# Optimization experiments

Measured on AMD Instinct MI355X. Metric: run time of the kernel, lower is better.

Reference implementation:

```python
import jax, jax.numpy as jnp
import numpy as np

B, N, M = 1, 3000, 3000        # surface points, query points
K = N + M                       # nodes per graph
IN, HID, H, OUT = 3, 64, 4, 2   # in_channels, hidden_channels, heads, out_channels
RADIUS2 = 0.05 ** 2
NEG_SLOPE = 0.2
NEG_INF = jnp.float32(-1e9)


def setup_inputs() -> dict:
    key = jax.random.key(0)
    ks = jax.random.split(key, 12)
    s1 = 1.0 / np.sqrt(IN)
    s2 = 1.0 / np.sqrt(H * HID)
    return {
        "pos": jax.random.uniform(ks[0], (B, 3, N), dtype=jnp.float32),
        "pos_non_manifold": jax.random.uniform(ks[1], (B, 3, M), dtype=jnp.float32),
        # GAT layer 1: lin weight, attention vectors (per head), bias
        "W1": jax.random.normal(ks[2], (IN, H * HID), dtype=jnp.float32) * s1,
        "a_src1": jax.random.normal(ks[3], (H, HID), dtype=jnp.float32) * s2,
        "a_dst1": jax.random.normal(ks[4], (H, HID), dtype=jnp.float32) * s2,
        "b1": jnp.zeros((H * HID,), dtype=jnp.float32),
        # GAT layer 2
        "W2": jax.random.normal(ks[5], (H * HID, H * HID), dtype=jnp.float32) * s2,
        "a_src2": jax.random.normal(ks[6], (H, HID), dtype=jnp.float32) * s2,
        "a_dst2": jax.random.normal(ks[7], (H, HID), dtype=jnp.float32) * s2,
        "b2": jnp.zeros((H * HID,), dtype=jnp.float32),
        # final fc
        "fc_w": jax.random.normal(ks[8], (H * HID, OUT), dtype=jnp.float32) * s2,
        "fc_b": jnp.zeros((OUT,), dtype=jnp.float32),
    }


def _gat_layer(x, mask, W, a_src, a_dst, b):
    # x: [B,K,Fin]; mask: [B,K,K] (mask[b,i,j] True if edge j->i, symmetric, incl. diag)
    h = (x @ W).reshape(x.shape[0], x.shape[1], H, HID)        # [B,K,H,C]
    es = jnp.einsum('bjhc,hc->bjh', h, a_src)                   # source score
    ed = jnp.einsum('bihc,hc->bih', h, a_dst)                   # destination score
    e = ed[:, :, None, :] + es[:, None, :, :]                   # [B,i,j,H]
    e = jnp.where(e >= 0, e, NEG_SLOPE * e)                     # LeakyReLU(0.2)
    e = jnp.where(mask[..., None], e, NEG_INF)
    alpha = jax.nn.softmax(e, axis=2)                           # softmax over sources j
    out = jnp.einsum('bijh,bjhc->bihc', alpha, h)               # [B,K,H,C]
    return out.reshape(x.shape[0], x.shape[1], H * HID) + b


def reference(pos, pos_non_manifold, W1, a_src1, a_dst1, b1,
              W2, a_src2, a_dst2, b2, fc_w, fc_b):
    # cat along point dim then transpose -> [B, K, 3]
    pts = jnp.concatenate([pos, pos_non_manifold], axis=2).transpose(0, 2, 1)
    # squared cdist via gram trick (avoids [B,K,K,3] intermediate)
    sq = jnp.sum(pts * pts, axis=-1)                            # [B,K]
    d2 = sq[:, :, None] + sq[:, None, :] - 2.0 * jnp.einsum('bid,bjd->bij', pts, pts)
    mask = d2 < RADIUS2                                         # adjacency (block-diag per batch)
    x = jax.nn.relu(_gat_layer(pts, mask, W1, a_src1, a_dst1, b1))
    x = jax.nn.relu(_gat_layer(x, mask, W2, a_src2, a_dst2, b2))
    x = x @ fc_w + fc_b                                         # [B,K,OUT]
    # original: x[:, num_points:].reshape(B, OUT, 3000) with num_points = M
    logits = x[:, M:].reshape(pts.shape[0], OUT, 3000)
    return logits
```

## Files before the change

### kernel.cpp

```cpp
#include <hip/hip_runtime.h>

#define NPTS   3000
#define MPTS   3000
#define KNODES 6000
#define HEADS  4
#define FDIM   256
#define OUTC   2
#define R2     0.0025f
#define NSLOPE 0.2f
#define MAXNBR 64
#define RPB    8

#define GDIM   16
#define NCELL  4096
#define CAP    16
#define POISON 0xAAAAAAAAu

#define OFF_ES2  0
#define OFF_ED2  24000
#define OFF_H2   48000
#define OFF_END  1584000

typedef const float __attribute__((address_space(1)))* gas_fp;
typedef float __attribute__((address_space(3)))*       las_fp;

__device__ __forceinline__ float wsum(float v) {
#pragma unroll
    for (int off = 32; off; off >>= 1) v += __shfl_xor(v, off, 64);
    return v;
}

__global__ void k_grid(const float* __restrict__ pos, const float* __restrict__ pnm,
                       unsigned* __restrict__ cellcnt, float4* __restrict__ bucket) {
    int i = blockIdx.x * 256 + threadIdx.x;
    if (i >= KNODES) return;
    float x, y, z;
    if (i < NPTS) { x = pos[i]; y = pos[NPTS + i]; z = pos[2 * NPTS + i]; }
    else { int q = i - NPTS; x = pnm[q]; y = pnm[MPTS + q]; z = pnm[2 * MPTS + q]; }
    int cx = min((int)(x * 16.f), 15);
    int cy = min((int)(y * 16.f), 15);
    int cz = min((int)(z * 16.f), 15);
    int cell = (cz << 8) | (cy << 4) | cx;
    unsigned slot = atomicAdd(&cellcnt[cell], 1u) - POISON;
    if (slot < CAP)
        bucket[cell * CAP + slot] = make_float4(x, y, z, __int_as_float(i));
}

__global__ __launch_bounds__(256) void k_main(
        const float* __restrict__ pos, const float* __restrict__ pnm,
        const float* __restrict__ W1, const float* __restrict__ as1,
        const float* __restrict__ ad1, const float* __restrict__ b1,
        const float* __restrict__ W2, const float* __restrict__ as2,
        const float* __restrict__ ad2,
        const unsigned* __restrict__ cellcnt, const float4* __restrict__ bucket,
        float* __restrict__ h2, float* __restrict__ es2, float* __restrict__ ed2,
        int* __restrict__ cnt, int* __restrict__ idx) {
    __shared__ __align__(16) float smem[8192];
    __shared__ int   s_cnt[RPB];
    __shared__ float s_u[HEADS][3], s_v[HEADS][3];
    __shared__ float s_q[RPB][HEADS][3];
    __shared__ __align__(16) float xs[RPB][FDIM];
    int*   s_idx = (int*)smem;
    float* s_nx  = smem + 512;
    float* s_ny  = smem + 1024;
    float* s_nz  = smem + 1536;
    const int t = threadIdx.x;
    const int lane = t & 63;
    const int wv = t >> 6;
    const int i0 = blockIdx.x * RPB;
    if (t < RPB) s_cnt[t] = 0;

    const float w1a = W1[t], w1b = W1[FDIM + t], w1c = W1[2 * FDIM + t];
    {
        const float asv = as1[t], adv = ad1[t];
        float u0 = wsum(w1a * asv), u1 = wsum(w1b * asv), u2 = wsum(w1c * asv);
        float v0 = wsum(w1a * adv), v1 = wsum(w1b * adv), v2 = wsum(w1c * adv);
        if (lane == 0) {
            int h = t >> 6;
            s_u[h][0] = u0; s_u[h][1] = u1; s_u[h][2] = u2;
            s_v[h][0] = v0; s_v[h][1] = v1; s_v[h][2] = v2;
        }
    }

    const float* base = (i0 < NPTS) ? pos : pnm;
    const int ib = (i0 < NPTS) ? i0 : i0 - NPTS;
    float xi[RPB], yi[RPB], zi[RPB], si[RPB];
#pragma unroll
    for (int r = 0; r < RPB; ++r) {
        float px = base[ib + r], py = base[NPTS + ib + r], pz = base[2 * NPTS + ib + r];
        xi[r] = px; yi[r] = py; zi[r] = pz;
        si[r] = __fadd_rn(__fadd_rn(__fmul_rn(px, px), __fmul_rn(py, py)),
                          __fmul_rn(pz, pz));
    }
    __syncthreads();

    {
        const int r = t >> 5, l32 = t & 31;
        if (l32 < 27) {
            int cx = min((int)(xi[r] * 16.f), 15);
            int cy = min((int)(yi[r] * 16.f), 15);
            int cz = min((int)(zi[r] * 16.f), 15);
            int dx = l32 % 3 - 1, dy = (l32 / 3) % 3 - 1, dz = l32 / 9 - 1;
            int nx_ = cx + dx, ny_ = cy + dy, nz_ = cz + dz;
            if (((nx_ | ny_ | nz_) >= 0) && nx_ < 16 && ny_ < 16 && nz_ < 16) {
                int cell = (nz_ << 8) | (ny_ << 4) | nx_;
                unsigned n = min(cellcnt[cell] - POISON, (unsigned)CAP);
                for (unsigned e = 0; e < n; ++e) {
                    float4 pj = bucket[cell * CAP + e];
                    float sj = __fadd_rn(__fadd_rn(__fmul_rn(pj.x, pj.x),
                                                   __fmul_rn(pj.y, pj.y)),
                                         __fmul_rn(pj.z, pj.z));
                    float dot = __fadd_rn(__fadd_rn(__fmul_rn(xi[r], pj.x),
                                                    __fmul_rn(yi[r], pj.y)),
                                          __fmul_rn(zi[r], pj.z));
                    float d2 = __fsub_rn(__fadd_rn(si[r], sj), __fmul_rn(2.0f, dot));
                    if (d2 < R2) {
                        int p = atomicAdd(&s_cnt[r], 1);
                        if (p < MAXNBR) {
                            s_idx[p * RPB + r] = __float_as_int(pj.w);
                            s_nx[p * RPB + r] = pj.x;
                            s_ny[p * RPB + r] = pj.y;
                            s_nz[p * RPB + r] = pj.z;
                        }
                    }
                }
            }
        }
    }
    __syncthreads();
    if (i0 >= NPTS) {
        if (t < RPB) cnt[i0 + t] = min(s_cnt[t], MAXNBR);
#pragma unroll
        for (int r = 0; r < RPB; ++r) {
            int c = min(s_cnt[r], MAXNBR);
            if (t < c) idx[(i0 + r) * MAXNBR + t] = s_idx[t * RPB + r];
        }
    }

    if (t < 64) {
        const int pr = (t & 31) >> 2, h = t & 3;
        const int c = min(s_cnt[pr], MAXNBR);
        const float u0 = s_u[h][0], u1 = s_u[h][1], u2 = s_u[h][2];
        const float dsum = fmaf(xi[pr], s_v[h][0],
                           fmaf(yi[pr], s_v[h][1], zi[pr] * s_v[h][2]));
        float m = -1e30f;
        for (int jl = 0; jl < c; ++jl) {
            float e = dsum + fmaf(s_nx[jl * RPB + pr], u0,
                             fmaf(s_ny[jl * RPB + pr], u1, s_nz[jl * RPB + pr] * u2));
            e = (e >= 0.f) ? e : NSLOPE * e;
            m = fmaxf(m, e);
        }
        float S = 0.f, q0 = 0.f, q1 = 0.f, q2 = 0.f;
        for (int jl = 0; jl < c; ++jl) {
            float xj = s_nx[jl * RPB + pr], yj = s_ny[jl * RPB + pr],
                  zj = s_nz[jl * RPB + pr];
            float e = dsum + fmaf(xj, u0, fmaf(yj, u1, zj * u2));
            e = (e >= 0.f) ? e : NSLOPE * e;
            float a = __expf(e - m);
            S += a;
            q0 = fmaf(a, xj, q0); q1 = fmaf(a, yj, q1); q2 = fmaf(a, zj, q2);
        }
        if (t < 32) {
            float inv = 1.f / S;
            s_q[pr][h][0] = q0 * inv;
            s_q[pr][h][1] = q1 * inv;
            s_q[pr][h][2] = q2 * inv;
        }
    }
    __syncthreads();

    {
        const float b1v = b1[t];
        const int h = t >> 6;
#pragma unroll
        for (int r = 0; r < RPB; ++r) {
            float q0 = s_q[r][h][0], q1 = s_q[r][h][1], q2 = s_q[r][h][2];
            float v = fmaf(q0, w1a, fmaf(q1, w1b, q2 * w1c)) + b1v;
            xs[r][t] = fmaxf(v, 0.f);
        }
    }

    {
        const int tl = t & 127, halfb = t >> 7;
        const int rbase = halfb * 4;
        const float2* wbuf2 = (const float2*)smem;
        float acc0[4], acc1[4];
#pragma unroll
        for (int r = 0; r < 4; ++r) { acc0[r] = 0.f; acc1[r] = 0.f; }
#pragma unroll 1
        for (int kb = 0; kb < 8; ++kb) {
            __syncthreads();
            {
                const float* gsrc = W2 + kb * 8192;
#pragma unroll
                for (int q = 0; q < 8; ++q) {
                    const int seg = wv * 8 + q;
                    __builtin_amdgcn_global_load_lds(
                        (gas_fp)(gsrc + seg * 256 + lane * 4),
                        (las_fp)(smem + seg * 256),
                        16, 0, 0);
                }
            }
            __syncthreads();
#pragma unroll
            for (int k4l = 0; k4l < 8; ++k4l) {
                const int k4 = (kb << 3) + k4l;
                float2 w0 = wbuf2[(4 * k4l + 0) * 128 + tl];
                float2 w1 = wbuf2[(4 * k4l + 1) * 128 + tl];
                float2 w2 = wbuf2[(4 * k4l + 2) * 128 + tl];
                float2 w3 = wbuf2[(4 * k4l + 3) * 128 + tl];
#pragma unroll
                for (int r = 0; r < 4; ++r) {
                    float4 xv = ((const float4*)xs[rbase + r])[k4];
                    acc0[r] = fmaf(xv.x, w0.x, fmaf(xv.y, w1.x,
                              fmaf(xv.z, w2.x, fmaf(xv.w, w3.x, acc0[r]))));
                    acc1[r] = fmaf(xv.x, w0.y, fmaf(xv.y, w1.y,
                              fmaf(xv.z, w2.y, fmaf(xv.w, w3.y, acc1[r]))));
                }
            }
        }
        const int c0 = 2 * tl;
#pragma unroll
        for (int r = 0; r < 4; ++r) {
            int row = i0 + rbase + r;
            *(float2*)&h2[(size_t)row * FDIM + c0] = make_float2(acc0[r], acc1[r]);
        }
        const float as0 = as2[c0], as1v = as2[c0 + 1];
        const float ad0 = ad2[c0], ad1v = ad2[c0 + 1];
        const int hh = tl >> 5;
#pragma unroll
        for (int r = 0; r < 4; ++r) {
            int row = i0 + rbase + r;
            float s = fmaf(acc0[r], as0, acc1[r] * as1v);
            float d = fmaf(acc0[r], ad0, acc1[r] * ad1v);
#pragma unroll
            for (int off = 16; off; off >>= 1) {
                s += __shfl_down(s, off, 64);
                d += __shfl_down(d, off, 64);
            }
            if ((lane & 31) == 0) {
                es2[row * HEADS + hh] = s;
                ed2[row * HEADS + hh] = d;
            }
        }
    }
}

__global__ void k_agg2fc(const float* __restrict__ h, const float* __restrict__ es,
                         const float* __restrict__ ed, const int* __restrict__ cnt,
                         const int* __restrict__ idx, const float* __restrict__ bias,
                         const float* __restrict__ fw, const float* __restrict__ fb,
                         float* __restrict__ out) {
    __shared__ int   s_idx[MAXNBR];
    __shared__ float s_e[MAXNBR * HEADS];
    __shared__ float s_ed[HEADS];
    __shared__ float s_red[8];
    int q = blockIdx.x;
    int i = MPTS + q;
    int t = threadIdx.x;
    int c = cnt[i];
    if (t < c) s_idx[t] = idx[i * MAXNBR + t];
    if (t < HEADS) s_ed[t] = ed[i * HEADS + t];
    __syncthreads();
    if (t < c * HEADS) {
        int jl = t >> 2, hh = t & 3;
        float e = s_ed[hh] + es[s_idx[jl] * HEADS + hh];
        e = (e >= 0.f) ? e : NSLOPE * e;
        s_e[jl * HEADS + hh] = e;
    }
    __syncthreads();
    int hh = t >> 6;
    float m = -1e30f;
    for (int jl = 0; jl < c; ++jl) m = fmaxf(m, s_e[jl * HEADS + hh]);
    float ssum = 0.f, acc = 0.f;
    for (int jl = 0; jl < c; ++jl) {
        float p = __expf(s_e[jl * HEADS + hh] - m);
        ssum += p;
        acc = fmaf(p, h[s_idx[jl] * FDIM + t], acc);
    }
    float v = fmaxf(acc / ssum + bias[t], 0.f);
    float p0 = v * fw[t * OUTC + 0];
    float p1 = v * fw[t * OUTC + 1];
    for (int off = 32; off; off >>= 1) {
        p0 += __shfl_down(p0, off, 64);
        p1 += __shfl_down(p1, off, 64);
    }
    if ((t & 63) == 0) {
        s_red[(t >> 6) * 2 + 0] = p0;
        s_red[(t >> 6) * 2 + 1] = p1;
    }
    __syncthreads();
    if (t == 0) {
        out[q * OUTC + 0] = s_red[0] + s_red[2] + s_red[4] + s_red[6] + fb[0];
        out[q * OUTC + 1] = s_red[1] + s_red[3] + s_red[5] + s_red[7] + fb[1];
    }
}

extern "C" void kernel_launch(void* const* d_in, const int* in_sizes, int n_in,
                              void* d_out, int out_size, void* d_ws, size_t ws_size,
                              hipStream_t stream) {
    const float* pos   = (const float*)d_in[0];
    const float* pnm   = (const float*)d_in[1];
    const float* W1    = (const float*)d_in[2];
    const float* asrc1 = (const float*)d_in[3];
    const float* adst1 = (const float*)d_in[4];
    const float* b1    = (const float*)d_in[5];
    const float* W2    = (const float*)d_in[6];
    const float* asrc2 = (const float*)d_in[7];
    const float* adst2 = (const float*)d_in[8];
    const float* b2    = (const float*)d_in[9];
    const float* fcw   = (const float*)d_in[10];
    const float* fcb   = (const float*)d_in[11];
    float* out = (float*)d_out;

    float* w    = (float*)d_ws;
    float* es2  = w + OFF_ES2;
    float* ed2  = w + OFF_ED2;
    float* h2   = w + OFF_H2;
    int* nbr_cnt = (int*)((char*)d_ws + (size_t)4 * OFF_END);
    int* nbr_idx = nbr_cnt + KNODES;
    unsigned* cellcnt = (unsigned*)(nbr_idx + (size_t)KNODES * MAXNBR);
    float4* bucket = (float4*)(cellcnt + NCELL);

    k_grid<<<(KNODES + 255) / 256, 256, 0, stream>>>(pos, pnm, cellcnt, bucket);
    k_main<<<KNODES / RPB, 256, 0, stream>>>(pos, pnm, W1, asrc1, adst1, b1,
                                             W2, asrc2, adst2, cellcnt, bucket,
                                             h2, es2, ed2, nbr_cnt, nbr_idx);
    k_agg2fc<<<MPTS, FDIM, 0, stream>>>(h2, es2, ed2, nbr_cnt, nbr_idx, b2,
                                        fcw, fcb, out);
}
```

Before: 115.7 us.

## Double-buffer W2 tiles in LDS and trim per-row register and work

The layer-2 GEMM now streams W2 in 16 smaller tiles through two LDS buffers. The next tile is prefetched with global_load_lds while the current one is consumed, and the first tile load overlaps the layer-1 projection. Point coordinates are re-read from global memory where needed instead of holding 8-row register arrays, which lowers register pressure. The softmax stage runs on 32 threads instead of 64, and surface-point blocks skip computing the unused destination score. In exchange the loop has more iterations and barriers, and the coordinates are loaded from global memory more than once.

```diff
diff --git a/kernel.cpp b/kernel.cpp
--- a/kernel.cpp
+++ b/kernel.cpp
@@ -84,22 +84,20 @@
 
     const float* base = (i0 < NPTS) ? pos : pnm;
     const int ib = (i0 < NPTS) ? i0 : i0 - NPTS;
-    float xi[RPB], yi[RPB], zi[RPB], si[RPB];
-#pragma unroll
-    for (int r = 0; r < RPB; ++r) {
-        float px = base[ib + r], py = base[NPTS + ib + r], pz = base[2 * NPTS + ib + r];
-        xi[r] = px; yi[r] = py; zi[r] = pz;
-        si[r] = __fadd_rn(__fadd_rn(__fmul_rn(px, px), __fmul_rn(py, py)),
-                          __fmul_rn(pz, pz));
-    }
     __syncthreads();
 
     {
         const int r = t >> 5, l32 = t & 31;
         if (l32 < 27) {
-            int cx = min((int)(xi[r] * 16.f), 15);
-            int cy = min((int)(yi[r] * 16.f), 15);
-            int cz = min((int)(zi[r] * 16.f), 15);
+            const float px = base[ib + r];
+            const float py = base[NPTS + ib + r];
+            const float pz = base[2 * NPTS + ib + r];
+            const float sir = __fadd_rn(__fadd_rn(__fmul_rn(px, px),
+                                                  __fmul_rn(py, py)),
+                                        __fmul_rn(pz, pz));
+            int cx = min((int)(px * 16.f), 15);
+            int cy = min((int)(py * 16.f), 15);
+            int cz = min((int)(pz * 16.f), 15);
             int dx = l32 % 3 - 1, dy = (l32 / 3) % 3 - 1, dz = l32 / 9 - 1;
             int nx_ = cx + dx, ny_ = cy + dy, nz_ = cz + dz;
             if (((nx_ | ny_ | nz_) >= 0) && nx_ < 16 && ny_ < 16 && nz_ < 16) {
@@ -110,10 +108,10 @@
                     float sj = __fadd_rn(__fadd_rn(__fmul_rn(pj.x, pj.x),
                                                    __fmul_rn(pj.y, pj.y)),
                                          __fmul_rn(pj.z, pj.z));
-                    float dot = __fadd_rn(__fadd_rn(__fmul_rn(xi[r], pj.x),
-                                                    __fmul_rn(yi[r], pj.y)),
-                                          __fmul_rn(zi[r], pj.z));
-                    float d2 = __fsub_rn(__fadd_rn(si[r], sj), __fmul_rn(2.0f, dot));
+                    float dot = __fadd_rn(__fadd_rn(__fmul_rn(px, pj.x),
+                                                    __fmul_rn(py, pj.y)),
+                                          __fmul_rn(pz, pj.z));
+                    float d2 = __fsub_rn(__fadd_rn(sir, sj), __fmul_rn(2.0f, dot));
                     if (d2 < R2) {
                         int p = atomicAdd(&s_cnt[r], 1);
                         if (p < MAXNBR) {
@@ -137,12 +135,15 @@
         }
     }
 
-    if (t < 64) {
-        const int pr = (t & 31) >> 2, h = t & 3;
+    if (t < 32) {
+        const int pr = t >> 2, h = t & 3;
+        const float px = base[ib + pr];
+        const float py = base[NPTS + ib + pr];
+        const float pz = base[2 * NPTS + ib + pr];
         const int c = min(s_cnt[pr], MAXNBR);
         const float u0 = s_u[h][0], u1 = s_u[h][1], u2 = s_u[h][2];
-        const float dsum = fmaf(xi[pr], s_v[h][0],
-                           fmaf(yi[pr], s_v[h][1], zi[pr] * s_v[h][2]));
+        const float dsum = fmaf(px, s_v[h][0],
+                           fmaf(py, s_v[h][1], pz * s_v[h][2]));
         float m = -1e30f;
         for (int jl = 0; jl < c; ++jl) {
             float e = dsum + fmaf(s_nx[jl * RPB + pr], u0,
@@ -160,15 +161,26 @@
             S += a;
             q0 = fmaf(a, xj, q0); q1 = fmaf(a, yj, q1); q2 = fmaf(a, zj, q2);
         }
-        if (t < 32) {
-            float inv = 1.f / S;
-            s_q[pr][h][0] = q0 * inv;
-            s_q[pr][h][1] = q1 * inv;
-            s_q[pr][h][2] = q2 * inv;
-        }
-    }
-    __syncthreads();
-
+        float inv = 1.f / S;
+        s_q[pr][h][0] = q0 * inv;
+        s_q[pr][h][1] = q1 * inv;
+        s_q[pr][h][2] = q2 * inv;
+    }
+    __syncthreads();
+
+    float* const bufA = smem;
+    float* const bufB = smem + 4096;
+    {
+        const float* gsrc = W2;
+#pragma unroll
+        for (int q = 0; q < 4; ++q) {
+            const int seg = wv * 4 + q;
+            __builtin_amdgcn_global_load_lds(
+                (gas_fp)(gsrc + seg * 256 + lane * 4),
+                (las_fp)(bufA + seg * 256),
+                16, 0, 0);
+        }
+    }
     {
         const float b1v = b1[t];
         const int h = t >> 6;
@@ -179,32 +191,32 @@
             xs[r][t] = fmaxf(v, 0.f);
         }
     }
-
-    {
-        const int tl = t & 127, halfb = t >> 7;
-        const int rbase = halfb * 4;
-        const float2* wbuf2 = (const float2*)smem;
+    __syncthreads();
+
+    {
+        const int tl = t & 127;
+        const int rbase = (t >> 7) * 4;
         float acc0[4], acc1[4];
 #pragma unroll
         for (int r = 0; r < 4; ++r) { acc0[r] = 0.f; acc1[r] = 0.f; }
 #pragma unroll 1
-        for (int kb = 0; kb < 8; ++kb) {
-            __syncthreads();
-            {
-                const float* gsrc = W2 + kb * 8192;
-#pragma unroll
-                for (int q = 0; q < 8; ++q) {
-                    const int seg = wv * 8 + q;
+        for (int kb = 0; kb < 16; ++kb) {
+            if (kb < 15) {
+                const float* gsrc = W2 + (kb + 1) * 4096;
+                float* dbuf = (kb & 1) ? bufA : bufB;
+#pragma unroll
+                for (int q = 0; q < 4; ++q) {
+                    const int seg = wv * 4 + q;
                     __builtin_amdgcn_global_load_lds(
                         (gas_fp)(gsrc + seg * 256 + lane * 4),
-                        (las_fp)(smem + seg * 256),
+                        (las_fp)(dbuf + seg * 256),
                         16, 0, 0);
                 }
             }
-            __syncthreads();
-#pragma unroll
-            for (int k4l = 0; k4l < 8; ++k4l) {
-                const int k4 = (kb << 3) + k4l;
+            const float2* wbuf2 = (const float2*)((kb & 1) ? bufB : bufA);
+#pragma unroll
+            for (int k4l = 0; k4l < 4; ++k4l) {
+                const int k4 = (kb << 2) + k4l;
                 float2 w0 = wbuf2[(4 * k4l + 0) * 128 + tl];
                 float2 w1 = wbuf2[(4 * k4l + 1) * 128 + tl];
                 float2 w2 = wbuf2[(4 * k4l + 2) * 128 + tl];
@@ -218,6 +230,7 @@
                               fmaf(xv.z, w2.y, fmaf(xv.w, w3.y, acc1[r]))));
                 }
             }
+            if (kb < 15) __syncthreads();
         }
         const int c0 = 2 * tl;
 #pragma unroll
@@ -226,21 +239,33 @@
             *(float2*)&h2[(size_t)row * FDIM + c0] = make_float2(acc0[r], acc1[r]);
         }
         const float as0 = as2[c0], as1v = as2[c0 + 1];
-        const float ad0 = ad2[c0], ad1v = ad2[c0 + 1];
         const int hh = tl >> 5;
-#pragma unroll
-        for (int r = 0; r < 4; ++r) {
-            int row = i0 + rbase + r;
-            float s = fmaf(acc0[r], as0, acc1[r] * as1v);
-            float d = fmaf(acc0[r], ad0, acc1[r] * ad1v);
-#pragma unroll
-            for (int off = 16; off; off >>= 1) {
-                s += __shfl_down(s, off, 64);
-                d += __shfl_down(d, off, 64);
-            }
-            if ((lane & 31) == 0) {
-                es2[row * HEADS + hh] = s;
-                ed2[row * HEADS + hh] = d;
+        if (i0 >= NPTS) {
+            const float ad0 = ad2[c0], ad1v = ad2[c0 + 1];
+#pragma unroll
+            for (int r = 0; r < 4; ++r) {
+                int row = i0 + rbase + r;
+                float s = fmaf(acc0[r], as0, acc1[r] * as1v);
+                float d = fmaf(acc0[r], ad0, acc1[r] * ad1v);
+#pragma unroll
+                for (int off = 16; off; off >>= 1) {
+                    s += __shfl_down(s, off, 64);
+                    d += __shfl_down(d, off, 64);
+                }
+                if ((lane & 31) == 0) {
+                    es2[row * HEADS + hh] = s;
+                    ed2[row * HEADS + hh] = d;
+                }
+            }
+        } else {
+#pragma unroll
+            for (int r = 0; r < 4; ++r) {
+                int row = i0 + rbase + r;
+                float s = fmaf(acc0[r], as0, acc1[r] * as1v);
+#pragma unroll
+                for (int off = 16; off; off >>= 1)
+                    s += __shfl_down(s, off, 64);
+                if ((lane & 31) == 0) es2[row * HEADS + hh] = s;
             }
         }
     }
```

Measured after the change: 114.5 us (median of 2 runs). About the same (-1.1%).
